# Optimization experiments

Hardware: AMD Instinct MI355X
Metric: run time of the kernel (lower is better)

The kernel has to match this reference:

```python
import jax, jax.numpy as jnp
import numpy as np

B, N, D, H = 8, 512, 1024, 16
HD = D // H
NI = 4          # num_instances == num_instances_per_batch
MAXI = 16       # max_instances
SCALE = HD ** -0.5


def _rms(t, w, eps=1e-6):
    return t * jax.lax.rsqrt(jnp.mean(t * t, axis=-1, keepdims=True) + eps) * w


def _lin(t, W, b):
    return t @ W + b


def _heads(t):
    b, n = t.shape[0], t.shape[1]
    return t.reshape(b, n, H, HD).transpose(0, 2, 1, 3)  # [b, H, n, hd]


def setup_inputs() -> dict:
    key = jax.random.key(0)
    ks = iter(jax.random.split(key, 16))

    def w(shape):
        return jax.random.normal(next(ks), shape, dtype=jnp.float32) * 0.02

    return {
        "x": jax.random.normal(next(ks), (B, N, D), dtype=jnp.float32),
        "instance_mask": jax.random.uniform(next(ks), (B, N, NI), dtype=jnp.float32),
        "Wq": w((D, D)), "bq": jnp.zeros((D,), jnp.float32),
        "Wk": w((D, D)), "bk": jnp.zeros((D,), jnp.float32),
        "Wv": w((D, D)), "bv": jnp.zeros((D,), jnp.float32),
        "Wo": w((D, D)), "bo": jnp.zeros((D,), jnp.float32),
        "Wiq": w((D, D)), "biq": jnp.zeros((D,), jnp.float32),
        "Wik": w((D, D)), "bik": jnp.zeros((D,), jnp.float32),
        "instance_embed": w((1, MAXI, D)),
        "qnorm_w": jnp.ones((HD,), jnp.float32),
        "knorm_w": jnp.ones((HD,), jnp.float32),
        "num_instances": NI,
        "num_instances_per_batch": NI,
    }


def reference(x, instance_mask, Wq, bq, Wk, bk, Wv, bv, Wo, bo,
              Wiq, biq, Wik, bik, instance_embed, qnorm_w, knorm_w,
              num_instances, num_instances_per_batch):
    # QKV projections + per-head QK-RMSNorm
    q = _rms(_heads(_lin(x, Wq, bq)), qnorm_w)   # [B,H,N,hd]
    k = _rms(_heads(_lin(x, Wk, bk)), knorm_w)
    v = _heads(_lin(x, Wv, bv))
    ni = num_instances                           # == num_instances_per_batch here,
    G = B // num_instances_per_batch             # so no leftover self-attn sub-branch;
    # (the module's initial global attention output is overwritten by this branch)
    qg = q.reshape(G, ni, H, N, HD)
    kg = k.reshape(G, ni, H, N, HD).transpose(0, 2, 1, 3, 4).reshape(G, H, ni * N, HD)
    vg = v.reshape(G, ni, H, N, HD).transpose(0, 2, 1, 3, 4).reshape(G, H, ni * N, HD)
    scores = jnp.einsum('gihnd,ghmd->gihnm', qg, kg) * SCALE  # [G,ni,H,N,ni*N]
    p = jax.nn.softmax(scores, axis=-1)
    og = jnp.einsum('gihnm,ghmd->gihnd', p, vg)
    out = og.reshape(B, H, N, HD).transpose(0, 2, 1, 3).reshape(B, N, D)
    # instance-embedding gate
    inst_feat = jnp.einsum('bnk,kd->bnd', instance_mask, instance_embed[0, :ni])
    iq = _heads(_lin(out, Wiq, biq))
    ik = _heads(_lin(inst_feat, Wik, bik))
    # mean over heads folded into the einsum (same math as mean of per-head scores)
    inst_attn = jax.nn.sigmoid(jnp.einsum('bhnd,bhmd->bnm', iq, ik) * (SCALE / H))
    gate = 1.0 + jnp.mean(inst_attn, axis=-1, keepdims=True)  # [B,N,1]
    return _lin(out * gate, Wo, bo)
```

## Files before the change

kernel.cpp:

```cpp
#include <hip/hip_runtime.h>
#include <cmath>

#define B_   8
#define N_   512
#define D_   1024
#define H_   16
#define HD_  64
#define NI_  4
#define BN_  (B_*N_)
#define KVLEN (NI_*N_)

typedef __attribute__((ext_vector_type(8)))  short  bf16x8;
typedef __attribute__((ext_vector_type(8)))  __bf16 bf16x8_t;
typedef __attribute__((ext_vector_type(16))) float  f32x16;
typedef __attribute__((ext_vector_type(4)))  short  s16x4;
typedef __attribute__((ext_vector_type(2)))  unsigned u32x2;

__device__ __forceinline__ short bf16_rn(float x) {
  unsigned u = __float_as_uint(x);
  unsigned r = (u + 0x7FFFu + ((u >> 16) & 1u)) >> 16;
  return (short)r;
}

__device__ __forceinline__ f32x16 mfma_bf16(bf16x8 a, bf16x8 b, f32x16 c) {
  return __builtin_amdgcn_mfma_f32_32x32x16_bf16(
      __builtin_bit_cast(bf16x8_t, a), __builtin_bit_cast(bf16x8_t, b), c, 0, 0, 0);
}

#define GLOAD16(gp, lp) __builtin_amdgcn_global_load_lds( \
  (const __attribute__((address_space(1))) unsigned*)(gp), \
  (__attribute__((address_space(3))) unsigned*)(lp), 16, 0, 0)

__device__ __forceinline__ long tiled_off(int row, int k) {
  return ((((long)(row >> 7) * 128 + (k >> 3)) * 128 + (row & 127)) * 8 + (k & 7));
}

__device__ __forceinline__ void xcd_swizzle(int& bx, int& by, int& bz) {
  const int gx = gridDim.x, gy = gridDim.y;
  const int nwg = gx * gy * gridDim.z;
  const int lin = blockIdx.x + gx * (blockIdx.y + gy * blockIdx.z);
  const int swz = (lin & 7) * (nwg >> 3) + (lin >> 3);
  bx = swz % gx;
  const int rest = swz / gx;
  by = rest % gy;
  bz = rest / gy;
}

__global__ __launch_bounds__(256) void wsplitAll(
    const float* __restrict__ Wq, const float* __restrict__ Wk,
    const float* __restrict__ Wv, const float* __restrict__ Wo,
    const float* __restrict__ x,
    short* __restrict__ QKVh, short* __restrict__ WoH,
    short* __restrict__ Xh)
{
  const int z = blockIdx.z;
  const int t  = threadIdx.x;
  if (z >= 4) {
    const int rowB = (z - 4) * 1024 + blockIdx.y * 64;
    const int colB = blockIdx.x * 64;
    const int r0 = t >> 4;
    const int c4 = t & 15;
    #pragma unroll
    for (int i = 0; i < 4; i++) {
      const int row = rowB + r0 + i * 16;
      float4 v = *(const float4*)&x[(long)row * D_ + colB + c4 * 4];
      short h[4];
      h[0] = bf16_rn(v.x);  h[1] = bf16_rn(v.y);
      h[2] = bf16_rn(v.z);  h[3] = bf16_rn(v.w);
      *(s16x4*)&Xh[tiled_off(row, colB + c4 * 4)] = *(s16x4*)h;
    }
    return;
  }
  __shared__ float tile[64][65];
  const float* W = (z == 0) ? Wq : (z == 1) ? Wk : (z == 2) ? Wv : Wo;
  const int kb = blockIdx.y * 64;
  const int cb = blockIdx.x * 64;
  const int r0 = t >> 4;
  const int c4 = t & 15;
  #pragma unroll
  for (int i = 0; i < 4; i++) {
    const int r = r0 + i * 16;
    *(float4*)&tile[r][c4 * 4] = *(const float4*)&W[(long)(kb + r) * D_ + cb + c4 * 4];
  }
  __syncthreads();
  #pragma unroll
  for (int i = 0; i < 4; i++) {
    const int c = r0 + i * 16;
    short hi[4];
    #pragma unroll
    for (int e = 0; e < 4; e++)
      hi[e] = bf16_rn(tile[c4 * 4 + e][c]);
    if (z < 3)
      *(s16x4*)&QKVh[tiled_off(z * D_ + cb + c, kb + c4 * 4)] = *(s16x4*)hi;
    else
      *(s16x4*)&WoH[tiled_off(cb + c, kb + c4 * 4)] = *(s16x4*)hi;
  }
}

__global__ __launch_bounds__(256) void fprep_p(
    const float* __restrict__ Wik, const float* __restrict__ emb,
    float* __restrict__ F4p)
{
  const int d  = blockIdx.x * 256 + threadIdx.x;
  const int eb = blockIdx.y;
  float s0 = 0, s1 = 0, s2 = 0, s3 = 0;
  for (int e = eb * 16; e < eb * 16 + 16; e++) {
    const float w = Wik[(long)e * D_ + d];
    s0 = fmaf(emb[e], w, s0);
    s1 = fmaf(emb[D_ + e], w, s1);
    s2 = fmaf(emb[2 * D_ + e], w, s2);
    s3 = fmaf(emb[3 * D_ + e], w, s3);
  }
  float* p = F4p + (long)eb * 4 * D_;
  p[d] = s0;  p[D_ + d] = s1;  p[2 * D_ + d] = s2;  p[3 * D_ + d] = s3;
}

__global__ __launch_bounds__(256) void freduce(
    const float* __restrict__ F4p, float* __restrict__ F4)
{
  const int i = blockIdx.x * 256 + threadIdx.x;
  float s = 0.f;
  #pragma unroll
  for (int eb = 0; eb < 64; eb++) s += F4p[(long)eb * 4096 + i];
  F4[i] = s;
}

__global__ __launch_bounds__(256) void hprep2(
    const float* __restrict__ Wiq, const float* __restrict__ F4,
    const float* __restrict__ bik, const float* __restrict__ biq,
    float* __restrict__ H5)
{
  __shared__ float red[4][5];
  const int t = threadIdx.x;
  const int blk = blockIdx.x;
  float s[5] = {0.f, 0.f, 0.f, 0.f, 0.f};
  const float* vr = (blk < 1024) ? Wiq + (long)blk * D_ : biq;
  for (int e = t; e < D_; e += 256) {
    const float w = vr[e];
    s[0] = fmaf(w, F4[e], s[0]);
    s[1] = fmaf(w, F4[D_ + e], s[1]);
    s[2] = fmaf(w, F4[2 * D_ + e], s[2]);
    s[3] = fmaf(w, F4[3 * D_ + e], s[3]);
    s[4] = fmaf(w, bik[e], s[4]);
  }
  #pragma unroll
  for (int j = 0; j < 5; j++)
    #pragma unroll
    for (int m = 1; m < 64; m <<= 1) s[j] += __shfl_xor(s[j], m);
  const int w64 = t >> 6, lane = t & 63;
  if (lane == 0)
    #pragma unroll
    for (int j = 0; j < 5; j++) red[w64][j] = s[j];
  __syncthreads();
  if (t < 5)
    H5[(long)blk * 5 + t] = red[0][t] + red[1][t] + red[2][t] + red[3][t];
}

template<int MODE>
__global__ __launch_bounds__(256) void mfgemm2(
    const short* __restrict__ Ahi, const short* __restrict__ Bhi,
    const float* __restrict__ b0, const float* __restrict__ b1,
    const float* __restrict__ b2,
    float* __restrict__ C, short* __restrict__ Vout,
    short* __restrict__ Kout, const float* __restrict__ knw,
    int bBlk, long sC, const float* __restrict__ gate_in)
{
  __shared__ short lds[2][2][4096];
  const int t = threadIdx.x, w = t >> 6, lane = t & 63;
  int bx, by, bz;
  xcd_swizzle(bx, by, bz);
  const int rowBase = by * 128;
  const int colBase = bx * 128;
  const long aoff = (long)by * 131072;
  const long boff = (long)(bz * bBlk + bx) * 131072;

  const int op = w >> 1, half = w & 1;
  const short* mySrc = op ? Bhi + boff : Ahi + aoff;

  auto stage = [&](int buf, int tt) {
    const short* g = mySrc + ((long)tt * 512 + half * 256 + lane) * 8;
    #pragma unroll
    for (int i = 0; i < 4; i++)
      GLOAD16(g + i * 512, &lds[buf][op][(half * 256 + i * 64) * 8]);
  };

  const int wr = w >> 1, wc = w & 1;
  const int lrow = lane & 31, lk = lane >> 5;

  f32x16 acc[2][2] = {};

  auto compute = [&](int buf) {
    #pragma unroll
    for (int kh = 0; kh < 2; kh++) {
      const int kq = 2 * kh + lk;
      bf16x8 ah[2], bh[2];
      #pragma unroll
      for (int m = 0; m < 2; m++)
        ah[m] = *(const bf16x8*)&lds[buf][0][(kq * 128 + wr * 64 + m * 32 + lrow) * 8];
      #pragma unroll
      for (int n = 0; n < 2; n++)
        bh[n] = *(const bf16x8*)&lds[buf][1][(kq * 128 + wc * 64 + n * 32 + lrow) * 8];
      #pragma unroll
      for (int m = 0; m < 2; m++)
        #pragma unroll
        for (int n = 0; n < 2; n++)
          acc[m][n] = mfma_bf16(ah[m], bh[n], acc[m][n]);
    }
  };

  const int NT = 32;
  stage(0, 0);
  for (int tt = 0; tt < NT - 1; ++tt) {
    stage((tt + 1) & 1, tt + 1);
    asm volatile("s_waitcnt vmcnt(4)" ::: "memory");
    __builtin_amdgcn_s_barrier();
    __builtin_amdgcn_sched_barrier(0);
    compute(tt & 1);
    __builtin_amdgcn_s_barrier();
  }
  asm volatile("s_waitcnt vmcnt(0)" ::: "memory");
  __builtin_amdgcn_s_barrier();
  __builtin_amdgcn_sched_barrier(0);
  compute((NT - 1) & 1);

  const float* bias = (bz == 1) ? b1 : (bz == 2) ? b2 : b0;
  float bcol[2];
  #pragma unroll
  for (int n = 0; n < 2; n++)
    bcol[n] = bias[colBase + wc * 64 + n * 32 + lrow];

  if (MODE == 6 && bz == 2) {
    #pragma unroll
    for (int m = 0; m < 2; m++)
      #pragma unroll
      for (int r = 0; r < 16; r++) {
        const int row = rowBase + wr * 64 + m * 32 + (r & 3) + 8 * (r >> 2) + 4 * lk;
        const int bb = row >> 9, g = bb >> 2;
        const int kv = (bb & 3) * 512 + (row & 511);
        const int tile = kv >> 5, vkv = kv & 31;
        #pragma unroll
        for (int n = 0; n < 2; n++) {
          const int col = colBase + wc * 64 + n * 32 + lrow;
          const int h = col >> 6, dl = col & 63;
          const long idx = ((long)(g * H_ + h) * 64 + tile) * 2048
                         + dl * 32 + (((vkv >> 3) ^ ((dl >> 1) & 3)) * 8) + (vkv & 7);
          Vout[idx] = bf16_rn(acc[m][n][r] + bcol[n]);
        }
      }
    return;
  }

  if (MODE == 6 && bz == 1) {
    const float kw0 = knw[lrow];
    const float kw1 = knw[32 + lrow];
    const int h = (colBase + wc * 64) >> 6;
    #pragma unroll
    for (int m = 0; m < 2; m++)
      #pragma unroll
      for (int r = 0; r < 16; r++) {
        const int row = rowBase + wr * 64 + m * 32 + (r & 3) + 8 * (r >> 2) + 4 * lk;
        const int bb = row >> 9, g = bb >> 2;
        const int mkv = (bb & 3) * 512 + (row & 511);
        const float v0 = acc[m][0][r] + bcol[0];
        const float v1 = acc[m][1][r] + bcol[1];
        float ks2 = v0 * v0 + v1 * v1;
        ks2 += __shfl_xor(ks2, 1);
        ks2 += __shfl_xor(ks2, 2);
        ks2 += __shfl_xor(ks2, 4);
        ks2 += __shfl_xor(ks2, 8);
        ks2 += __shfl_xor(ks2, 16);
        const float kr = rsqrtf(ks2 * (1.f / 64.f) + 1e-6f);
        const long base = ((long)(g * H_ + h) * KVLEN + mkv) * 64;
        const int d0 = lrow, d1 = 32 + lrow;
        Kout[base + (((d0 >> 3) ^ (mkv & 7)) << 3) + (d0 & 7)] = bf16_rn(v0 * kr * kw0);
        Kout[base + (((d1 >> 3) ^ (mkv & 7)) << 3) + (d1 & 7)] = bf16_rn(v1 * kr * kw1);
      }
    return;
  }

  float* Cb = C + (long)bz * sC;
  #pragma unroll
  for (int m = 0; m < 2; m++) {
    #pragma unroll
    for (int r = 0; r < 16; r++) {
      const int row = rowBase + wr * 64 + m * 32 + (r & 3) + 8 * (r >> 2) + 4 * lk;
      float g = 1.f;
      if (MODE == 2) g = gate_in[row];
      #pragma unroll
      for (int n = 0; n < 2; n++) {
        const int col = colBase + wc * 64 + n * 32 + lrow;
        Cb[(long)row * D_ + col] = acc[m][n][r] * g + bcol[n];
      }
    }
  }
}

__global__ __launch_bounds__(256) void attn3(
    const float* __restrict__ q, const short* __restrict__ Knb,
    const short* __restrict__ Vtb, const float* __restrict__ qnw,
    float* __restrict__ opart, float* __restrict__ lpart)
{
  int qb, h, bz;
  xcd_swizzle(qb, h, bz);
  const int b  = bz >> 1, s = bz & 1;
  const int g  = b >> 2;
  const int t  = threadIdx.x;
  const int w  = t >> 6;
  const int lane = t & 63;
  const int l31 = lane & 31, hi = lane >> 5;

  __shared__ short Kt[2][2048];
  __shared__ short Vt[2][2048];

  const int qrow = qb * 128 + w * 32 + l31;
  const float* qp = q + ((long)b * N_ + qrow) * D_ + h * HD_ + hi * 8;
  float qv[4][8];
  float ss = 0.f;
  #pragma unroll
  for (int c = 0; c < 4; c++) {
    *(float4*)&qv[c][0] = *(const float4*)&qp[c * 16];
    *(float4*)&qv[c][4] = *(const float4*)&qp[c * 16 + 4];
    #pragma unroll
    for (int j = 0; j < 8; j++) ss += qv[c][j] * qv[c][j];
  }
  ss += __shfl_xor(ss, 32);
  const float qr = rsqrtf(ss * (1.f / 64.f) + 1e-6f) * 0.1803368801111244f;
  bf16x8 qf[4];
  #pragma unroll
  for (int c = 0; c < 4; c++)
    #pragma unroll
    for (int j = 0; j < 8; j++)
      qf[c][j] = bf16_rn(qv[c][j] * qr * qnw[c * 16 + hi * 8 + j]);

  const short* Kg = Knb + (long)(g * H_ + h) * KVLEN * 64 + (long)s * 32 * 2048;
  const short* Vg = Vtb + (long)(g * H_ + h) * 64 * 2048 + (long)s * 32 * 2048;

  auto stage = [&](int buf, int i) {
    GLOAD16(Kg + (long)i * 2048 + t * 8, &Kt[buf][w * 512]);
    GLOAD16(Vg + (long)i * 2048 + t * 8, &Vt[buf][w * 512]);
  };

  f32x16 oacc[2] = {};
  float l = 0.f;

  stage(0, 0);
  for (int i = 0; i < 32; ++i) {
    const int buf = i & 1;
    if (i + 1 < 32) {
      stage(buf ^ 1, i + 1);
      asm volatile("s_waitcnt vmcnt(2)" ::: "memory");
    } else {
      asm volatile("s_waitcnt vmcnt(0)" ::: "memory");
    }
    __builtin_amdgcn_s_barrier();
    __builtin_amdgcn_sched_barrier(0);

    f32x16 sc = {};
    #pragma unroll
    for (int c = 0; c < 4; c++) {
      bf16x8 kfr = *(const bf16x8*)&Kt[buf][l31 * 64 + (((2 * c + hi) * 8) ^ ((l31 & 7) << 3))];
      sc = mfma_bf16(kfr, qf[c], sc);
    }
    float p[16];
    #pragma unroll
    for (int r = 0; r < 16; r++) {
      p[r] = exp2f(sc[r]);
      l += p[r];
    }
    unsigned wd[8];
    #pragma unroll
    for (int i2 = 0; i2 < 8; i2++)
      asm("v_cvt_pk_bf16_f32 %0, %1, %2" : "=v"(wd[i2]) : "v"(p[2 * i2]), "v"(p[2 * i2 + 1]));
    u32x2 r0 = __builtin_amdgcn_permlane32_swap(wd[0], wd[2], false, false);
    u32x2 r1 = __builtin_amdgcn_permlane32_swap(wd[1], wd[3], false, false);
    u32x2 r2 = __builtin_amdgcn_permlane32_swap(wd[4], wd[6], false, false);
    u32x2 r3 = __builtin_amdgcn_permlane32_swap(wd[5], wd[7], false, false);
    int4 f0 = { (int)r0.x, (int)r1.x, (int)r0.y, (int)r1.y };
    int4 f1 = { (int)r2.x, (int)r3.x, (int)r2.y, (int)r3.y };
    #pragma unroll
    for (int n = 0; n < 2; n++) {
      const int d = n * 32 + l31;
      const int fd = (d >> 1) & 3;
      bf16x8 v0 = *(const bf16x8*)&Vt[buf][d * 32 + ((hi ^ fd) * 8)];
      bf16x8 v1 = *(const bf16x8*)&Vt[buf][d * 32 + (((2 | hi) ^ fd) * 8)];
      oacc[n] = mfma_bf16(__builtin_bit_cast(bf16x8, f0), v0, oacc[n]);
      oacc[n] = mfma_bf16(__builtin_bit_cast(bf16x8, f1), v1, oacc[n]);
    }
    __builtin_amdgcn_s_barrier();
  }

  l += __shfl_xor(l, 32);
  #pragma unroll
  for (int r = 0; r < 16; r++) {
    const int qg = qb * 128 + w * 32 + (r & 3) + 8 * (r >> 2) + 4 * hi;
    float* op = opart + ((long)s * BN_ + b * N_ + qg) * D_ + h * HD_ + l31;
    op[0]  = oacc[0][r];
    op[32] = oacc[1][r];
  }
  if (hi == 0)
    lpart[((long)s * BN_ + b * N_ + qb * 128 + w * 32 + l31) * H_ + h] = l;
}

__global__ __launch_bounds__(256) void attn_reduce2(
    const float* __restrict__ opart, const float* __restrict__ lpart,
    const float* __restrict__ H5, const float* __restrict__ mask,
    short* __restrict__ ohi, float* __restrict__ gate)
{
  __shared__ float red[4][5];
  __shared__ float Gs[5];
  __shared__ float sred[4];
  const int t = threadIdx.x;
  const int row = blockIdx.x;
  const int bb = row >> 9;
  const int col = t * 4;
  const int h   = col >> 6;
  const float l = lpart[(long)row * H_ + h] + lpart[((long)BN_ + row) * H_ + h];
  const float inv = 1.f / l;
  float4 a = *(const float4*)&opart[(long)row * D_ + col];
  float4 b = *(const float4*)&opart[((long)BN_ + row) * D_ + col];
  float o4[4] = { (a.x + b.x) * inv, (a.y + b.y) * inv,
                  (a.z + b.z) * inv, (a.w + b.w) * inv };
  short hh[4];
  hh[0] = bf16_rn(o4[0]);  hh[1] = bf16_rn(o4[1]);
  hh[2] = bf16_rn(o4[2]);  hh[3] = bf16_rn(o4[3]);
  *(s16x4*)&ohi[tiled_off(row, col)] = *(s16x4*)hh;
  float s[5] = {0.f, 0.f, 0.f, 0.f, 0.f};
  #pragma unroll
  for (int cc = 0; cc < 4; cc++) {
    const float* hp = &H5[(long)(col + cc) * 5];
    #pragma unroll
    for (int j = 0; j < 5; j++) s[j] = fmaf(o4[cc], hp[j], s[j]);
  }
  #pragma unroll
  for (int j = 0; j < 5; j++)
    #pragma unroll
    for (int m = 1; m < 64; m <<= 1) s[j] += __shfl_xor(s[j], m);
  const int w64 = t >> 6, lane = t & 63;
  if (lane == 0)
    #pragma unroll
    for (int j = 0; j < 5; j++) red[w64][j] = s[j];
  __syncthreads();
  if (t < 5) Gs[t] = red[0][t] + red[1][t] + red[2][t] + red[3][t] + H5[5120 + t];
  __syncthreads();
  const float g0 = Gs[0], g1 = Gs[1], g2 = Gs[2], g3 = Gs[3], g4 = Gs[4];
  const float sc = 0.125f / 16.f;
  const float* mrow = mask + (long)bb * N_ * NI_;
  float sg = 0.f;
  #pragma unroll
  for (int q = 0; q < 2; q++) {
    const float4 mk = *(const float4*)&mrow[(t * 2 + q) * 4];
    const float z = fmaf(g0, mk.x, fmaf(g1, mk.y, fmaf(g2, mk.z, fmaf(g3, mk.w, g4))));
    sg += 1.f / (1.f + __expf(-z * sc));
  }
  #pragma unroll
  for (int m = 1; m < 64; m <<= 1) sg += __shfl_xor(sg, m);
  if (lane == 0) sred[w64] = sg;
  __syncthreads();
  if (t == 0)
    gate[row] = 1.f + (sred[0] + sred[1] + sred[2] + sred[3]) * (1.f / 512.f);
}

extern "C" void kernel_launch(void* const* d_in, const int* in_sizes, int n_in,
                              void* d_out, int out_size, void* d_ws, size_t ws_size,
                              hipStream_t stream)
{
  const float* x    = (const float*)d_in[0];
  const float* mask = (const float*)d_in[1];
  const float* Wq   = (const float*)d_in[2];
  const float* bq   = (const float*)d_in[3];
  const float* Wk   = (const float*)d_in[4];
  const float* bk   = (const float*)d_in[5];
  const float* Wv   = (const float*)d_in[6];
  const float* bv   = (const float*)d_in[7];
  const float* Wo   = (const float*)d_in[8];
  const float* bo   = (const float*)d_in[9];
  const float* Wiq  = (const float*)d_in[10];
  const float* biq  = (const float*)d_in[11];
  const float* Wik  = (const float*)d_in[12];
  const float* bik  = (const float*)d_in[13];
  const float* emb  = (const float*)d_in[14];
  const float* qnw  = (const float*)d_in[15];
  const float* knw  = (const float*)d_in[16];
  float* out = (float*)d_out;

  float* ws = (float*)d_ws;
  const size_t SZ = (size_t)BN_ * D_;
  float* qbuf = ws;
  float* opart = ws + SZ;
  short* ohi  = (short*)qbuf;
  short* Knb  = (short*)(ws + 3 * SZ);
  short* xhi  = (short*)(ws + 4 * SZ);
  short* Vtb  = xhi + SZ;
  short* Wbig_hi = (short*)(ws + 5 * SZ);
  short* Wbig_lo = Wbig_hi + (size_t)3 * D_ * D_;
  float* gate  = (float*)Wbig_hi;
  float* lpart = gate + BN_;
  short* WoH = Wbig_lo;
  float* F4  = (float*)(Wbig_lo + (size_t)D_ * D_);
  float* H5  = F4 + 4 * D_;
  float* F4p = H5 + 1025 * 5;

  const dim3 blk(256);

  fprep_p<<<dim3(4, 64), blk, 0, stream>>>(Wik, emb, F4p);
  freduce<<<dim3(16), blk, 0, stream>>>(F4p, F4);
  hprep2<<<dim3(1025), blk, 0, stream>>>(Wiq, F4, bik, biq, H5);

  wsplitAll<<<dim3(16, 16, 8), blk, 0, stream>>>(
      Wq, Wk, Wv, Wo, x, Wbig_hi, WoH, xhi);

  mfgemm2<6><<<dim3(8, 32, 3), blk, 0, stream>>>(
      xhi, Wbig_hi, bq, bk, bv,
      qbuf, Vtb, Knb, knw, 8, (long)SZ, nullptr);

  attn3<<<dim3(N_ / 128, H_, B_ * 2), blk, 0, stream>>>(
      qbuf, Knb, Vtb, qnw, opart, lpart);

  attn_reduce2<<<BN_, blk, 0, stream>>>(opart, lpart, H5, mask, ohi, gate);

  mfgemm2<2><<<dim3(8, 32, 1), blk, 0, stream>>>(
      ohi, WoH, bo, nullptr, nullptr,
      out, nullptr, nullptr, nullptr, 0, 0, gate);
}
```

Measured before the change: 182.8 us.

## Fuse Q RMSNorm into QKV GEMM epilogue and store Q and attention partials in bf16

```diff
diff --git a/kernel.cpp b/kernel.cpp
--- a/kernel.cpp
+++ b/kernel.cpp
@@ -20,6 +20,10 @@
   unsigned u = __float_as_uint(x);
   unsigned r = (u + 0x7FFFu + ((u >> 16) & 1u)) >> 16;
   return (short)r;
+}
+
+__device__ __forceinline__ float bf2f(short x) {
+  return __uint_as_float(((unsigned)(unsigned short)x) << 16);
 }
 
 __device__ __forceinline__ f32x16 mfma_bf16(bf16x8 a, bf16x8 b, f32x16 c) {
@@ -161,8 +165,9 @@
     const short* __restrict__ Ahi, const short* __restrict__ Bhi,
     const float* __restrict__ b0, const float* __restrict__ b1,
     const float* __restrict__ b2,
-    float* __restrict__ C, short* __restrict__ Vout,
-    short* __restrict__ Kout, const float* __restrict__ knw,
+    float* __restrict__ C, short* __restrict__ Qout,
+    short* __restrict__ Kout, short* __restrict__ Vout,
+    const float* __restrict__ qnw, const float* __restrict__ knw,
     int bBlk, long sC, const float* __restrict__ gate_in)
 {
   __shared__ short lds[2][2][4096];
@@ -229,23 +234,26 @@
   for (int n = 0; n < 2; n++)
     bcol[n] = bias[colBase + wc * 64 + n * 32 + lrow];
 
-  if (MODE == 6 && bz == 2) {
+  if (MODE == 6 && bz == 0) {
+    const float qw0 = qnw[lrow];
+    const float qw1 = qnw[32 + lrow];
+    const int col0 = colBase + wc * 64 + lrow;
     #pragma unroll
     for (int m = 0; m < 2; m++)
       #pragma unroll
       for (int r = 0; r < 16; r++) {
         const int row = rowBase + wr * 64 + m * 32 + (r & 3) + 8 * (r >> 2) + 4 * lk;
-        const int bb = row >> 9, g = bb >> 2;
-        const int kv = (bb & 3) * 512 + (row & 511);
-        const int tile = kv >> 5, vkv = kv & 31;
-        #pragma unroll
-        for (int n = 0; n < 2; n++) {
-          const int col = colBase + wc * 64 + n * 32 + lrow;
-          const int h = col >> 6, dl = col & 63;
-          const long idx = ((long)(g * H_ + h) * 64 + tile) * 2048
-                         + dl * 32 + (((vkv >> 3) ^ ((dl >> 1) & 3)) * 8) + (vkv & 7);
-          Vout[idx] = bf16_rn(acc[m][n][r] + bcol[n]);
-        }
+        const float v0 = acc[m][0][r] + bcol[0];
+        const float v1 = acc[m][1][r] + bcol[1];
+        float ss = v0 * v0 + v1 * v1;
+        ss += __shfl_xor(ss, 1);
+        ss += __shfl_xor(ss, 2);
+        ss += __shfl_xor(ss, 4);
+        ss += __shfl_xor(ss, 8);
+        ss += __shfl_xor(ss, 16);
+        const float qr = rsqrtf(ss * (1.f / 64.f) + 1e-6f) * 0.1803368801111244f;
+        Qout[(long)row * D_ + col0]      = bf16_rn(v0 * qr * qw0);
+        Qout[(long)row * D_ + col0 + 32] = bf16_rn(v1 * qr * qw1);
       }
     return;
   }
@@ -278,6 +286,27 @@
     return;
   }
 
+  if (MODE == 6 && bz == 2) {
+    #pragma unroll
+    for (int m = 0; m < 2; m++)
+      #pragma unroll
+      for (int r = 0; r < 16; r++) {
+        const int row = rowBase + wr * 64 + m * 32 + (r & 3) + 8 * (r >> 2) + 4 * lk;
+        const int bb = row >> 9, g = bb >> 2;
+        const int kv = (bb & 3) * 512 + (row & 511);
+        const int tile = kv >> 5, vkv = kv & 31;
+        #pragma unroll
+        for (int n = 0; n < 2; n++) {
+          const int col = colBase + wc * 64 + n * 32 + lrow;
+          const int h = col >> 6, dl = col & 63;
+          const long idx = ((long)(g * H_ + h) * 64 + tile) * 2048
+                         + dl * 32 + (((vkv >> 3) ^ ((dl >> 1) & 3)) * 8) + (vkv & 7);
+          Vout[idx] = bf16_rn(acc[m][n][r] + bcol[n]);
+        }
+      }
+    return;
+  }
+
   float* Cb = C + (long)bz * sC;
   #pragma unroll
   for (int m = 0; m < 2; m++) {
@@ -296,9 +325,9 @@
 }
 
 __global__ __launch_bounds__(256) void attn3(
-    const float* __restrict__ q, const short* __restrict__ Knb,
-    const short* __restrict__ Vtb, const float* __restrict__ qnw,
-    float* __restrict__ opart, float* __restrict__ lpart)
+    const short* __restrict__ q, const short* __restrict__ Knb,
+    const short* __restrict__ Vtb,
+    short* __restrict__ opart, float* __restrict__ lpart)
 {
   int qb, h, bz;
   xcd_swizzle(qb, h, bz);
@@ -313,24 +342,11 @@
   __shared__ short Vt[2][2048];
 
   const int qrow = qb * 128 + w * 32 + l31;
-  const float* qp = q + ((long)b * N_ + qrow) * D_ + h * HD_ + hi * 8;
-  float qv[4][8];
-  float ss = 0.f;
-  #pragma unroll
-  for (int c = 0; c < 4; c++) {
-    *(float4*)&qv[c][0] = *(const float4*)&qp[c * 16];
-    *(float4*)&qv[c][4] = *(const float4*)&qp[c * 16 + 4];
-    #pragma unroll
-    for (int j = 0; j < 8; j++) ss += qv[c][j] * qv[c][j];
-  }
-  ss += __shfl_xor(ss, 32);
-  const float qr = rsqrtf(ss * (1.f / 64.f) + 1e-6f) * 0.1803368801111244f;
+  const short* qp = q + ((long)b * N_ + qrow) * D_ + h * HD_ + hi * 8;
   bf16x8 qf[4];
   #pragma unroll
   for (int c = 0; c < 4; c++)
-    #pragma unroll
-    for (int j = 0; j < 8; j++)
-      qf[c][j] = bf16_rn(qv[c][j] * qr * qnw[c * 16 + hi * 8 + j]);
+    qf[c] = *(const bf16x8*)&qp[c * 16];
 
   const short* Kg = Knb + (long)(g * H_ + h) * KVLEN * 64 + (long)s * 32 * 2048;
   const short* Vg = Vtb + (long)(g * H_ + h) * 64 * 2048 + (long)s * 32 * 2048;
@@ -363,10 +379,10 @@
     }
     float p[16];
     #pragma unroll
-    for (int r = 0; r < 16; r++) {
+    for (int r = 0; r < 16; r++)
       p[r] = exp2f(sc[r]);
-      l += p[r];
-    }
+    l += ((((p[0] + p[1]) + (p[2] + p[3])) + ((p[4] + p[5]) + (p[6] + p[7])))
+       + (((p[8] + p[9]) + (p[10] + p[11])) + ((p[12] + p[13]) + (p[14] + p[15]))));
     unsigned wd[8];
     #pragma unroll
     for (int i2 = 0; i2 < 8; i2++)
@@ -393,16 +409,16 @@
   #pragma unroll
   for (int r = 0; r < 16; r++) {
     const int qg = qb * 128 + w * 32 + (r & 3) + 8 * (r >> 2) + 4 * hi;
-    float* op = opart + ((long)s * BN_ + b * N_ + qg) * D_ + h * HD_ + l31;
-    op[0]  = oacc[0][r];
-    op[32] = oacc[1][r];
+    short* op = opart + ((long)s * BN_ + b * N_ + qg) * D_ + h * HD_ + l31;
+    op[0]  = bf16_rn(oacc[0][r]);
+    op[32] = bf16_rn(oacc[1][r]);
   }
   if (hi == 0)
     lpart[((long)s * BN_ + b * N_ + qb * 128 + w * 32 + l31) * H_ + h] = l;
 }
 
 __global__ __launch_bounds__(256) void attn_reduce2(
-    const float* __restrict__ opart, const float* __restrict__ lpart,
+    const short* __restrict__ opart, const float* __restrict__ lpart,
     const float* __restrict__ H5, const float* __restrict__ mask,
     short* __restrict__ ohi, float* __restrict__ gate)
 {
@@ -416,10 +432,12 @@
   const int h   = col >> 6;
   const float l = lpart[(long)row * H_ + h] + lpart[((long)BN_ + row) * H_ + h];
   const float inv = 1.f / l;
-  float4 a = *(const float4*)&opart[(long)row * D_ + col];
-  float4 b = *(const float4*)&opart[((long)BN_ + row) * D_ + col];
-  float o4[4] = { (a.x + b.x) * inv, (a.y + b.y) * inv,
-                  (a.z + b.z) * inv, (a.w + b.w) * inv };
+  s16x4 a4 = *(const s16x4*)&opart[(long)row * D_ + col];
+  s16x4 b4 = *(const s16x4*)&opart[((long)BN_ + row) * D_ + col];
+  float o4[4];
+  #pragma unroll
+  for (int c = 0; c < 4; c++)
+    o4[c] = (bf2f(a4[c]) + bf2f(b4[c])) * inv;
   short hh[4];
   hh[0] = bf16_rn(o4[0]);  hh[1] = bf16_rn(o4[1]);
   hh[2] = bf16_rn(o4[2]);  hh[3] = bf16_rn(o4[3]);
@@ -485,9 +503,9 @@
 
   float* ws = (float*)d_ws;
   const size_t SZ = (size_t)BN_ * D_;
-  float* qbuf = ws;
-  float* opart = ws + SZ;
-  short* ohi  = (short*)qbuf;
+  short* Qnb  = (short*)ws;
+  short* ohi  = (short*)ws;
+  short* opart = (short*)(ws + SZ);
   short* Knb  = (short*)(ws + 3 * SZ);
   short* xhi  = (short*)(ws + 4 * SZ);
   short* Vtb  = xhi + SZ;
@@ -511,14 +529,14 @@
 
   mfgemm2<6><<<dim3(8, 32, 3), blk, 0, stream>>>(
       xhi, Wbig_hi, bq, bk, bv,
-      qbuf, Vtb, Knb, knw, 8, (long)SZ, nullptr);
+      nullptr, Qnb, Knb, Vtb, qnw, knw, 8, 0, nullptr);
 
   attn3<<<dim3(N_ / 128, H_, B_ * 2), blk, 0, stream>>>(
-      qbuf, Knb, Vtb, qnw, opart, lpart);
+      Qnb, Knb, Vtb, opart, lpart);
 
   attn_reduce2<<<BN_, blk, 0, stream>>>(opart, lpart, H5, mask, ohi, gate);
 
   mfgemm2<2><<<dim3(8, 32, 1), blk, 0, stream>>>(
       ohi, WoH, bo, nullptr, nullptr,
-      out, nullptr, nullptr, nullptr, 0, 0, gate);
-}
+      out, nullptr, nullptr, nullptr, nullptr, nullptr, 0, 0, gate);
+}
```

Result: no change. 179.9 us (-1.6%).
